# Optimization experiments

Measured on AMD Instinct MI355X. Metric: run time of the kernel, lower is better.

The kernel has to match this reference:

```python
import jax, jax.numpy as jnp
import numpy as np

HEAD = 8


def setup_inputs() -> dict:
    key0 = jax.random.key(0)
    ks = jax.random.split(key0, 16)
    B, K, RD, NH = 16, 1024, 1024, 1024
    s = 0.02
    inp = {
        "v": jax.random.normal(ks[0], (B, K, RD), jnp.float32),
        "key": jax.random.normal(ks[1], (B, K, RD), jnp.float32),
        "query": jax.random.normal(ks[2], (B, K, RD), jnp.float32),
        "mask": jax.random.randint(ks[3], (B, 1, 1, K), 0, 2).astype(bool),
        # FCNet([relation_dim, num_hid], act='') == Linear(relation_dim, num_hid)
        "Wq": jax.random.normal(ks[4], (RD, NH), jnp.float32) * s,
        "bq": jnp.zeros((NH,), jnp.float32),
        "Wk": jax.random.normal(ks[5], (RD, NH), jnp.float32) * s,
        "bk": jnp.zeros((NH,), jnp.float32),
        "Wv": jax.random.normal(ks[6], (RD, NH), jnp.float32) * s,
        "bv": jnp.zeros((NH,), jnp.float32),
        "Wm": jax.random.normal(ks[7], (NH, NH), jnp.float32) * s,
        "bm": jnp.zeros((NH,), jnp.float32),
    }
    return inp


def reference(v, key, query, mask, Wq, bq, Wk, bk, Wv, bv, Wm, bm):
    B, K, _ = v.shape
    NH = Wq.shape[1]
    dk = NH // HEAD

    def split_heads(x):  # [B,K,NH] -> [B,H,K,dk]
        return x.reshape(B, K, HEAD, dk).transpose(0, 2, 1, 3)

    q = split_heads(query @ Wq + bq)
    k = split_heads(key @ Wk + bk)
    vv = split_heads(v @ Wv + bv)

    scores = jnp.einsum("bhqd,bhkd->bhqk", q, k) / jnp.sqrt(jnp.float32(dk))
    scores = jnp.where(mask, jnp.float32(-1e9), scores)
    att = jax.nn.softmax(scores, axis=-1)  # dropout is identity at eval
    atted = jnp.einsum("bhqk,bhkd->bhqd", att, vv)
    atted = atted.transpose(0, 2, 1, 3).reshape(B, K, NH)
    atted = atted @ Wm + bm
    return atted, att
```

## Files before the change

### kernel.cpp

```cpp
#include <hip/hip_runtime.h>

typedef unsigned short u16;
typedef __attribute__((ext_vector_type(8))) short short8;
typedef __attribute__((ext_vector_type(4))) float floatx4;

#define MFMA16(a, b, c) __builtin_amdgcn_mfma_f32_16x16x32_bf16(a, b, c, 0, 0, 0)

#define BB 16
#define KK 1024
#define NH 1024
#define HD 8
#define DK 128
#define ATT_OFF 16777216

typedef const __attribute__((address_space(1))) unsigned gl_u32;
typedef __attribute__((address_space(3))) unsigned lds_u32;

__device__ __forceinline__ u16 f2bf(float x) {
  unsigned u = __builtin_bit_cast(unsigned, x);
  u += 0x7fffu + ((u >> 16) & 1u);
  return (u16)(u >> 16);
}

__device__ __forceinline__ void gload16(const u16* g, u16* l) {
  __builtin_amdgcn_global_load_lds((gl_u32*)g, (lds_u32*)l, 16, 0, 0);
}

__global__ __launch_bounds__(256) void cast_bf16x8(const float* __restrict__ in,
                                                   u16* __restrict__ out) {
  const size_t i = ((size_t)blockIdx.x * 256 + threadIdx.x) * 8;
  float4 f0 = *(const float4*)(in + i);
  float4 f1 = *(const float4*)(in + i + 4);
  union { u16 u[8]; uint4 v; } p;
  p.u[0] = f2bf(f0.x); p.u[1] = f2bf(f0.y); p.u[2] = f2bf(f0.z); p.u[3] = f2bf(f0.w);
  p.u[4] = f2bf(f1.x); p.u[5] = f2bf(f1.y); p.u[6] = f2bf(f1.z); p.u[7] = f2bf(f1.w);
  *(uint4*)(out + i) = p.v;
}

__global__ __launch_bounds__(256) void tr_w(const float* __restrict__ in,
                                            u16* __restrict__ out) {
  __shared__ u16 t[32][36];
  const int tid = threadIdx.x;
  const int bx = blockIdx.x * 32;
  const int by = blockIdx.y * 32;
  const int r = tid >> 3, c4 = (tid & 7) * 4;
  float4 f = *(const float4*)(in + (size_t)(by + r) * 1024 + bx + c4);
  t[r][c4 + 0] = f2bf(f.x);
  t[r][c4 + 1] = f2bf(f.y);
  t[r][c4 + 2] = f2bf(f.z);
  t[r][c4 + 3] = f2bf(f.w);
  __syncthreads();
  union { u16 u[4]; uint2 v; } p;
#pragma unroll
  for (int i = 0; i < 4; i++) p.u[i] = t[c4 + i][r];
  *(uint2*)(out + (size_t)(bx + r) * 1024 + by + c4) = p.v;
}

__global__ __launch_bounds__(256) void tr_head(const u16* __restrict__ vvb,
                                               u16* __restrict__ vvT) {
  __shared__ u16 t[32][36];
  const int tid = threadIdx.x;
  const int bh = blockIdx.z, b = bh >> 3, h = bh & 7;
  const int i0 = blockIdx.x * 32, d0 = blockIdx.y * 32;
  const int r = tid >> 3, c4 = (tid & 7) * 4;
  union { u16 u[4]; uint2 v; } p;
  p.v = *(const uint2*)(vvb + (size_t)(b * KK + i0 + r) * NH + h * DK + d0 + c4);
  t[r][c4 + 0] = p.u[0];
  t[r][c4 + 1] = p.u[1];
  t[r][c4 + 2] = p.u[2];
  t[r][c4 + 3] = p.u[3];
  __syncthreads();
#pragma unroll
  for (int i = 0; i < 4; i++) p.u[i] = t[c4 + i][r];
  *(uint2*)(vvT + (size_t)(bh * DK + d0 + r) * KK + i0 + c4) = p.v;
}

__global__ __launch_bounds__(256, 2) void gemm_bt(
    const u16* __restrict__ A, const u16* __restrict__ Bt,
    const float* __restrict__ bias, u16* __restrict__ Cb, float* __restrict__ Cf,
    int Kd, int ldc, long long aBatch, long long btBatch,
    long long cBatchB, long long cBatchH) {
  __shared__ __align__(16) u16 As[128 * 32];
  __shared__ __align__(16) u16 Bs[128 * 32];
  const int tid = threadIdx.x;
  const int z = blockIdx.z;

  int bxs = blockIdx.x, bys = blockIdx.y;
  if (gridDim.x == 8 && gridDim.y == 128 && gridDim.z == 1) {
    const int flat = blockIdx.x + 8 * blockIdx.y;
    const int xcd = flat & 7, idx = flat >> 3;
    const int nflat = xcd * 128 + idx;
    bxs = nflat & 7;
    bys = nflat >> 3;
  }
  const int nBase = bxs * 128;
  const int mBase = bys * 128;

  const u16* Ab = A + (size_t)z * aBatch;
  const u16* Bb = Bt + (size_t)z * btBatch;
  const size_t cOff = (size_t)(z >> 3) * cBatchB + (size_t)(z & 7) * cBatchH;

  const int wid = tid >> 6, lane = tid & 63;
  const int wm = (wid & 1) * 64, wn = (wid >> 1) * 64;
  const int lm = lane & 15, lq = lane >> 4;

  const int rIn = lane >> 2;
  const int sSlot = (lane & 3) * 8;
  u16* aDst0 = &As[(wid * 2 + 0) * 512];
  u16* aDst1 = &As[(wid * 2 + 1) * 512];
  u16* bDst0 = &Bs[(wid * 2 + 0) * 512];
  u16* bDst1 = &Bs[(wid * 2 + 1) * 512];
  const u16* aSrc0 = Ab + (size_t)(mBase + (wid * 2 + 0) * 16 + rIn) * Kd + sSlot;
  const u16* aSrc1 = Ab + (size_t)(mBase + (wid * 2 + 1) * 16 + rIn) * Kd + sSlot;
  const u16* bSrc0 = Bb + (size_t)(nBase + (wid * 2 + 0) * 16 + rIn) * Kd + sSlot;
  const u16* bSrc1 = Bb + (size_t)(nBase + (wid * 2 + 1) * 16 + rIn) * Kd + sSlot;

  floatx4 acc[4][4] = {};

  for (int k0 = 0; k0 < Kd; k0 += 32) {
    gload16(aSrc0 + k0, aDst0);
    gload16(aSrc1 + k0, aDst1);
    gload16(bSrc0 + k0, bDst0);
    gload16(bSrc1 + k0, bDst1);
    __syncthreads();

    short8 af[4], bfr[4];
#pragma unroll
    for (int t = 0; t < 4; t++) {
      af[t]  = *(const short8*)&As[(wm + t * 16 + lm) * 32 + lq * 8];
      bfr[t] = *(const short8*)&Bs[(wn + t * 16 + lm) * 32 + lq * 8];
    }
#pragma unroll
    for (int i = 0; i < 4; i++)
#pragma unroll
      for (int j = 0; j < 4; j++)
        acc[i][j] = MFMA16(af[i], bfr[j], acc[i][j]);
    __syncthreads();
  }

#pragma unroll
  for (int i = 0; i < 4; i++) {
    const int rowL = wm + i * 16 + lq * 4;
#pragma unroll
    for (int j = 0; j < 4; j++) {
      const int col = nBase + wn + j * 16 + lm;
      const float bval = bias ? bias[col] : 0.0f;
      const size_t base = cOff + (size_t)(mBase + rowL) * ldc + col;
#pragma unroll
      for (int r = 0; r < 4; r++) {
        const float v = acc[i][j][r] + bval;
        if (Cb) Cb[base + (size_t)r * ldc] = f2bf(v);
        if (Cf) Cf[base + (size_t)r * ldc] = v;
      }
    }
  }
}

__global__ __launch_bounds__(256, 2) void scores_softmax_pv(
    const u16* __restrict__ qb, const u16* __restrict__ kb,
    const int* __restrict__ mask, const u16* __restrict__ vvT,
    float* __restrict__ att, u16* __restrict__ atp) {
  __shared__ __align__(16) u16 p_lds[16 * 1024];
  u16* msk16 = p_lds;
  float* redM = (float*)&p_lds[1024];
  float* redS = (float*)&p_lds[1152];
  const int tid = threadIdx.x;

  const int flat = blockIdx.x + 64 * blockIdx.y;
  const int xcd = flat & 7, idx = flat >> 3;
  const int bh = xcd * 16 + (idx >> 6);
  const int rowBlk = idx & 63;

  const int b = bh >> 3, h = bh & 7;
  const int wid = tid >> 6, lane = tid & 63;
  const int lm = lane & 15, lq = lane >> 4;
  const int rowG = rowBlk * 16;

  {
    int4 m = *(const int4*)(mask + (size_t)b * KK + tid * 4);
    msk16[tid * 4 + 0] = (u16)(m.x != 0);
    msk16[tid * 4 + 1] = (u16)(m.y != 0);
    msk16[tid * 4 + 2] = (u16)(m.z != 0);
    msk16[tid * 4 + 3] = (u16)(m.w != 0);
  }

  short8 qf[4];
  const u16* qp = qb + (size_t)(b * KK + rowG + lm) * NH + h * DK + lq * 8;
#pragma unroll
  for (int ks = 0; ks < 4; ks++) qf[ks] = *(const short8*)(qp + ks * 32);

  floatx4 acc[16] = {};
  const u16* kpB = kb + (size_t)(b * KK + wid * 256 + lm) * NH + h * DK + lq * 8;
#pragma unroll
  for (int jt = 0; jt < 16; jt++) {
    const u16* kp = kpB + (size_t)jt * 16 * NH;
    short8 k0 = *(const short8*)(kp + 0);
    short8 k1 = *(const short8*)(kp + 32);
    short8 k2 = *(const short8*)(kp + 64);
    short8 k3 = *(const short8*)(kp + 96);
    floatx4 a = acc[jt];
    a = MFMA16(qf[0], k0, a);
    a = MFMA16(qf[1], k1, a);
    a = MFMA16(qf[2], k2, a);
    a = MFMA16(qf[3], k3, a);
    acc[jt] = a;
  }
  __syncthreads();

  const float scale = 0.08838834764831845f;
  float mrow[4] = {-3e38f, -3e38f, -3e38f, -3e38f};
#pragma unroll
  for (int jt = 0; jt < 16; jt++) {
    const int col = wid * 256 + jt * 16 + lm;
    const bool mk = msk16[col] != 0;
#pragma unroll
    for (int r = 0; r < 4; r++) {
      float s = mk ? -1e9f : acc[jt][r] * scale;
      acc[jt][r] = s;
      mrow[r] = fmaxf(mrow[r], s);
    }
  }
#pragma unroll
  for (int off = 1; off < 16; off <<= 1)
#pragma unroll
    for (int r = 0; r < 4; r++) mrow[r] = fmaxf(mrow[r], __shfl_xor(mrow[r], off));
  if (lm == 0) {
#pragma unroll
    for (int r = 0; r < 4; r++) redM[wid * 16 + lq * 4 + r] = mrow[r];
  }
  __syncthreads();
#pragma unroll
  for (int r = 0; r < 4; r++)
    mrow[r] = fmaxf(fmaxf(redM[0 + lq * 4 + r], redM[16 + lq * 4 + r]),
                    fmaxf(redM[32 + lq * 4 + r], redM[48 + lq * 4 + r]));

  float srow[4] = {0.f, 0.f, 0.f, 0.f};
#pragma unroll
  for (int jt = 0; jt < 16; jt++)
#pragma unroll
    for (int r = 0; r < 4; r++) {
      float e = __expf(acc[jt][r] - mrow[r]);
      acc[jt][r] = e;
      srow[r] += e;
    }
#pragma unroll
  for (int off = 1; off < 16; off <<= 1)
#pragma unroll
    for (int r = 0; r < 4; r++) srow[r] += __shfl_xor(srow[r], off);
  if (lm == 0) {
#pragma unroll
    for (int r = 0; r < 4; r++) redS[wid * 16 + lq * 4 + r] = srow[r];
  }
  __syncthreads();
#pragma unroll
  for (int r = 0; r < 4; r++) {
    float s = redS[0 + lq * 4 + r] + redS[16 + lq * 4 + r] +
              redS[32 + lq * 4 + r] + redS[48 + lq * 4 + r];
    srow[r] = 1.0f / s;
  }
  __syncthreads();

#pragma unroll
  for (int r = 0; r < 4; r++) {
    const int row = lq * 4 + r;
    float* attRow = att + ((size_t)bh * KK + rowG + row) * KK;
#pragma unroll
    for (int jt = 0; jt < 16; jt++) {
      const int col = wid * 256 + jt * 16 + lm;
      const float p = acc[jt][r] * srow[r];
      __builtin_nontemporal_store(p, attRow + col);
      p_lds[(row * 1024 + col) ^ ((row & 7) << 3)] = f2bf(p);
    }
  }
  __syncthreads();

  floatx4 pacc0 = {}, pacc1 = {}, pacc2 = {}, pacc3 = {};
  const u16* vBase = vvT + (size_t)bh * DK * KK + (size_t)(wid * 32 + lm) * KK + lq * 8;
#pragma unroll 4
  for (int k0 = 0; k0 < 512; k0 += 32) {
    short8 pfa = *(const short8*)&p_lds[(lm * 1024 + k0 + lq * 8) ^ ((lm & 7) << 3)];
    short8 pfb = *(const short8*)&p_lds[(lm * 1024 + 512 + k0 + lq * 8) ^ ((lm & 7) << 3)];
    short8 v0a = *(const short8*)(vBase + k0);
    short8 v1a = *(const short8*)(vBase + 16 * KK + k0);
    short8 v0b = *(const short8*)(vBase + 512 + k0);
    short8 v1b = *(const short8*)(vBase + 16 * KK + 512 + k0);
    pacc0 = MFMA16(pfa, v0a, pacc0);
    pacc1 = MFMA16(pfa, v1a, pacc1);
    pacc2 = MFMA16(pfb, v0b, pacc2);
    pacc3 = MFMA16(pfb, v1b, pacc3);
  }
  floatx4 o0 = pacc0 + pacc2;
  floatx4 o1 = pacc1 + pacc3;

#pragma unroll
  for (int r = 0; r < 4; r++) {
    const int row = rowG + lq * 4 + r;
    atp[(size_t)(b * KK + row) * NH + h * DK + wid * 32 + 0 + lm] = f2bf(o0[r]);
    atp[(size_t)(b * KK + row) * NH + h * DK + wid * 32 + 16 + lm] = f2bf(o1[r]);
  }
}

extern "C" void kernel_launch(void* const* d_in, const int* in_sizes, int n_in,
                              void* d_out, int out_size, void* d_ws, size_t ws_size,
                              hipStream_t stream) {
  const float* v     = (const float*)d_in[0];
  const float* key   = (const float*)d_in[1];
  const float* query = (const float*)d_in[2];
  const int*   mask  = (const int*)d_in[3];
  const float* Wq = (const float*)d_in[4];
  const float* bq = (const float*)d_in[5];
  const float* Wk = (const float*)d_in[6];
  const float* bk = (const float*)d_in[7];
  const float* Wv = (const float*)d_in[8];
  const float* bv = (const float*)d_in[9];
  const float* Wm = (const float*)d_in[10];
  const float* bm = (const float*)d_in[11];

  float* atted = (float*)d_out;
  float* att   = atted + (size_t)ATT_OFF;

  char* ws = (char*)d_ws;
  u16* qb   = (u16*)(ws + 0);
  u16* kb   = (u16*)(ws + 33554432ll);
  u16* vvb  = (u16*)(ws + 67108864ll);
  u16* vvT  = (u16*)(ws + 100663296ll);
  u16* atp  = (u16*)(ws + 134217728ll);
  u16* WqT  = (u16*)(ws + 167772160ll);
  u16* WkT  = (u16*)(ws + 169869312ll);
  u16* WvT  = (u16*)(ws + 171966464ll);
  u16* WmT  = (u16*)(ws + 174063616ll);

  u16* cq = (u16*)att;
  u16* ck = cq + 16777216;
  u16* cv = ck + 16777216;

  cast_bf16x8<<<8192, 256, 0, stream>>>(query, cq);
  cast_bf16x8<<<8192, 256, 0, stream>>>(key, ck);
  cast_bf16x8<<<8192, 256, 0, stream>>>(v, cv);

  tr_w<<<dim3(32, 32), 256, 0, stream>>>(Wq, WqT);
  tr_w<<<dim3(32, 32), 256, 0, stream>>>(Wk, WkT);
  tr_w<<<dim3(32, 32), 256, 0, stream>>>(Wv, WvT);
  tr_w<<<dim3(32, 32), 256, 0, stream>>>(Wm, WmT);

  gemm_bt<<<dim3(8, 128, 1), 256, 0, stream>>>(cq, WqT, bq, qb, nullptr,
                                               1024, 1024, 0, 0, 0, 0);
  gemm_bt<<<dim3(8, 128, 1), 256, 0, stream>>>(ck, WkT, bk, kb, nullptr,
                                               1024, 1024, 0, 0, 0, 0);
  gemm_bt<<<dim3(8, 128, 1), 256, 0, stream>>>(cv, WvT, bv, vvb, nullptr,
                                               1024, 1024, 0, 0, 0, 0);

  tr_head<<<dim3(32, 4, 128), 256, 0, stream>>>(vvb, vvT);

  scores_softmax_pv<<<dim3(64, 128), 256, 0, stream>>>(qb, kb, mask, vvT, att, atp);

  gemm_bt<<<dim3(8, 128, 1), 256, 0, stream>>>(atp, WmT, bm, nullptr, atted,
                                               1024, 1024, 0, 0, 0, 0);
}
```

Before: 1.337 ms.

## Double-buffer GEMM LDS, prefetch K/V fragments, batch cast and QKV launches

Double-buffers the GEMM shared-memory tiles so the next K-slice's global-to-LDS loads are issued before the current slice is consumed, leaving one barrier per iteration. The scores and PV phases now register-prefetch K and V fragments four steps ahead to hide global latency. The three cast kernels and the three QKV projection GEMMs are each merged into a single launch via a grid dimension, which cuts launch count and gives larger grids. The costs are doubled LDS use per GEMM block and higher register pressure from the prefetch buffers, which could reduce occupancy.

```diff
diff --git a/kernel.cpp b/kernel.cpp
--- a/kernel.cpp
+++ b/kernel.cpp
@@ -26,8 +26,12 @@
   __builtin_amdgcn_global_load_lds((gl_u32*)g, (lds_u32*)l, 16, 0, 0);
 }
 
-__global__ __launch_bounds__(256) void cast_bf16x8(const float* __restrict__ in,
-                                                   u16* __restrict__ out) {
+__global__ __launch_bounds__(256) void cast3_bf16x8(
+    const float* __restrict__ i0, const float* __restrict__ i1,
+    const float* __restrict__ i2, u16* __restrict__ o0, u16* __restrict__ o1,
+    u16* __restrict__ o2) {
+  const float* in = blockIdx.y == 0 ? i0 : (blockIdx.y == 1 ? i1 : i2);
+  u16* out = blockIdx.y == 0 ? o0 : (blockIdx.y == 1 ? o1 : o2);
   const size_t i = ((size_t)blockIdx.x * 256 + threadIdx.x) * 8;
   float4 f0 = *(const float4*)(in + i);
   float4 f1 = *(const float4*)(in + i + 4);
@@ -75,60 +79,46 @@
   *(uint2*)(vvT + (size_t)(bh * DK + d0 + r) * KK + i0 + c4) = p.v;
 }
 
-__global__ __launch_bounds__(256, 2) void gemm_bt(
-    const u16* __restrict__ A, const u16* __restrict__ Bt,
+__device__ __forceinline__ void gemm_body(
+    const u16* __restrict__ Ab, const u16* __restrict__ Bb,
     const float* __restrict__ bias, u16* __restrict__ Cb, float* __restrict__ Cf,
-    int Kd, int ldc, long long aBatch, long long btBatch,
-    long long cBatchB, long long cBatchH) {
-  __shared__ __align__(16) u16 As[128 * 32];
-  __shared__ __align__(16) u16 Bs[128 * 32];
+    const int Kd, const int ldc, const int nBase, const int mBase) {
+  __shared__ __align__(16) u16 As[2][128 * 32];
+  __shared__ __align__(16) u16 Bs[2][128 * 32];
   const int tid = threadIdx.x;
-  const int z = blockIdx.z;
-
-  int bxs = blockIdx.x, bys = blockIdx.y;
-  if (gridDim.x == 8 && gridDim.y == 128 && gridDim.z == 1) {
-    const int flat = blockIdx.x + 8 * blockIdx.y;
-    const int xcd = flat & 7, idx = flat >> 3;
-    const int nflat = xcd * 128 + idx;
-    bxs = nflat & 7;
-    bys = nflat >> 3;
-  }
-  const int nBase = bxs * 128;
-  const int mBase = bys * 128;
-
-  const u16* Ab = A + (size_t)z * aBatch;
-  const u16* Bb = Bt + (size_t)z * btBatch;
-  const size_t cOff = (size_t)(z >> 3) * cBatchB + (size_t)(z & 7) * cBatchH;
-
   const int wid = tid >> 6, lane = tid & 63;
   const int wm = (wid & 1) * 64, wn = (wid >> 1) * 64;
   const int lm = lane & 15, lq = lane >> 4;
-
   const int rIn = lane >> 2;
   const int sSlot = (lane & 3) * 8;
-  u16* aDst0 = &As[(wid * 2 + 0) * 512];
-  u16* aDst1 = &As[(wid * 2 + 1) * 512];
-  u16* bDst0 = &Bs[(wid * 2 + 0) * 512];
-  u16* bDst1 = &Bs[(wid * 2 + 1) * 512];
-  const u16* aSrc0 = Ab + (size_t)(mBase + (wid * 2 + 0) * 16 + rIn) * Kd + sSlot;
-  const u16* aSrc1 = Ab + (size_t)(mBase + (wid * 2 + 1) * 16 + rIn) * Kd + sSlot;
-  const u16* bSrc0 = Bb + (size_t)(nBase + (wid * 2 + 0) * 16 + rIn) * Kd + sSlot;
-  const u16* bSrc1 = Bb + (size_t)(nBase + (wid * 2 + 1) * 16 + rIn) * Kd + sSlot;
+
+  const u16* aS0 = Ab + (size_t)(mBase + (wid * 2 + 0) * 16 + rIn) * Kd + sSlot;
+  const u16* aS1 = Ab + (size_t)(mBase + (wid * 2 + 1) * 16 + rIn) * Kd + sSlot;
+  const u16* bS0 = Bb + (size_t)(nBase + (wid * 2 + 0) * 16 + rIn) * Kd + sSlot;
+  const u16* bS1 = Bb + (size_t)(nBase + (wid * 2 + 1) * 16 + rIn) * Kd + sSlot;
 
   floatx4 acc[4][4] = {};
 
+  gload16(aS0, &As[0][(wid * 2 + 0) * 512]);
+  gload16(aS1, &As[0][(wid * 2 + 1) * 512]);
+  gload16(bS0, &Bs[0][(wid * 2 + 0) * 512]);
+  gload16(bS1, &Bs[0][(wid * 2 + 1) * 512]);
+  __syncthreads();
+
+  int cur = 0;
   for (int k0 = 0; k0 < Kd; k0 += 32) {
-    gload16(aSrc0 + k0, aDst0);
-    gload16(aSrc1 + k0, aDst1);
-    gload16(bSrc0 + k0, bDst0);
-    gload16(bSrc1 + k0, bDst1);
-    __syncthreads();
-
+    const int nxt = cur ^ 1;
+    if (k0 + 32 < Kd) {
+      gload16(aS0 + k0 + 32, &As[nxt][(wid * 2 + 0) * 512]);
+      gload16(aS1 + k0 + 32, &As[nxt][(wid * 2 + 1) * 512]);
+      gload16(bS0 + k0 + 32, &Bs[nxt][(wid * 2 + 0) * 512]);
+      gload16(bS1 + k0 + 32, &Bs[nxt][(wid * 2 + 1) * 512]);
+    }
     short8 af[4], bfr[4];
 #pragma unroll
     for (int t = 0; t < 4; t++) {
-      af[t]  = *(const short8*)&As[(wm + t * 16 + lm) * 32 + lq * 8];
-      bfr[t] = *(const short8*)&Bs[(wn + t * 16 + lm) * 32 + lq * 8];
+      af[t]  = *(const short8*)&As[cur][(wm + t * 16 + lm) * 32 + lq * 8];
+      bfr[t] = *(const short8*)&Bs[cur][(wn + t * 16 + lm) * 32 + lq * 8];
     }
 #pragma unroll
     for (int i = 0; i < 4; i++)
@@ -136,6 +126,7 @@
       for (int j = 0; j < 4; j++)
         acc[i][j] = MFMA16(af[i], bfr[j], acc[i][j]);
     __syncthreads();
+    cur = nxt;
   }
 
 #pragma unroll
@@ -145,7 +136,7 @@
     for (int j = 0; j < 4; j++) {
       const int col = nBase + wn + j * 16 + lm;
       const float bval = bias ? bias[col] : 0.0f;
-      const size_t base = cOff + (size_t)(mBase + rowL) * ldc + col;
+      const size_t base = (size_t)(mBase + rowL) * ldc + col;
 #pragma unroll
       for (int r = 0; r < 4; r++) {
         const float v = acc[i][j][r] + bval;
@@ -154,6 +145,36 @@
       }
     }
   }
+}
+
+__device__ __forceinline__ int2 swz_grid() {
+  const int flat = blockIdx.x + 8 * blockIdx.y;
+  const int xcd = flat & 7, idx = flat >> 3;
+  const int nflat = xcd * 128 + idx;
+  return make_int2((nflat & 7) * 128, (nflat >> 3) * 128);
+}
+
+__global__ __launch_bounds__(256, 2) void gemm_bt(
+    const u16* __restrict__ A, const u16* __restrict__ Bt,
+    const float* __restrict__ bias, u16* __restrict__ Cb, float* __restrict__ Cf) {
+  int2 nm = swz_grid();
+  gemm_body(A, Bt, bias, Cb, Cf, 1024, 1024, nm.x, nm.y);
+}
+
+__global__ __launch_bounds__(256, 2) void gemm_qkv(
+    const u16* __restrict__ A0, const u16* __restrict__ A1,
+    const u16* __restrict__ A2, const u16* __restrict__ B0,
+    const u16* __restrict__ B1, const u16* __restrict__ B2,
+    const float* __restrict__ b0, const float* __restrict__ b1,
+    const float* __restrict__ b2, u16* __restrict__ C0, u16* __restrict__ C1,
+    u16* __restrict__ C2) {
+  const int z = blockIdx.z;
+  const u16* A = z == 0 ? A0 : (z == 1 ? A1 : A2);
+  const u16* B = z == 0 ? B0 : (z == 1 ? B1 : B2);
+  const float* bias = z == 0 ? b0 : (z == 1 ? b1 : b2);
+  u16* C = z == 0 ? C0 : (z == 1 ? C1 : C2);
+  int2 nm = swz_grid();
+  gemm_body(A, B, bias, C, nullptr, 1024, 1024, nm.x, nm.y);
 }
 
 __global__ __launch_bounds__(256, 2) void scores_softmax_pv(
@@ -191,18 +212,31 @@
 
   floatx4 acc[16] = {};
   const u16* kpB = kb + (size_t)(b * KK + wid * 256 + lm) * NH + h * DK + lq * 8;
+  short8 kf[4][4];
+#pragma unroll
+  for (int p = 0; p < 4; p++) {
+    const u16* kp = kpB + (size_t)p * 16 * NH;
+    kf[p][0] = *(const short8*)(kp + 0);
+    kf[p][1] = *(const short8*)(kp + 32);
+    kf[p][2] = *(const short8*)(kp + 64);
+    kf[p][3] = *(const short8*)(kp + 96);
+  }
 #pragma unroll
   for (int jt = 0; jt < 16; jt++) {
-    const u16* kp = kpB + (size_t)jt * 16 * NH;
-    short8 k0 = *(const short8*)(kp + 0);
-    short8 k1 = *(const short8*)(kp + 32);
-    short8 k2 = *(const short8*)(kp + 64);
-    short8 k3 = *(const short8*)(kp + 96);
+    const int slot = jt & 3;
+    short8 c0 = kf[slot][0], c1 = kf[slot][1], c2 = kf[slot][2], c3 = kf[slot][3];
+    if (jt + 4 < 16) {
+      const u16* kp = kpB + (size_t)(jt + 4) * 16 * NH;
+      kf[slot][0] = *(const short8*)(kp + 0);
+      kf[slot][1] = *(const short8*)(kp + 32);
+      kf[slot][2] = *(const short8*)(kp + 64);
+      kf[slot][3] = *(const short8*)(kp + 96);
+    }
     floatx4 a = acc[jt];
-    a = MFMA16(qf[0], k0, a);
-    a = MFMA16(qf[1], k1, a);
-    a = MFMA16(qf[2], k2, a);
-    a = MFMA16(qf[3], k3, a);
+    a = MFMA16(qf[0], c0, a);
+    a = MFMA16(qf[1], c1, a);
+    a = MFMA16(qf[2], c2, a);
+    a = MFMA16(qf[3], c3, a);
     acc[jt] = a;
   }
   __syncthreads();
@@ -276,18 +310,28 @@
 
   floatx4 pacc0 = {}, pacc1 = {}, pacc2 = {}, pacc3 = {};
   const u16* vBase = vvT + (size_t)bh * DK * KK + (size_t)(wid * 32 + lm) * KK + lq * 8;
-#pragma unroll 4
-  for (int k0 = 0; k0 < 512; k0 += 32) {
-    short8 pfa = *(const short8*)&p_lds[(lm * 1024 + k0 + lq * 8) ^ ((lm & 7) << 3)];
-    short8 pfb = *(const short8*)&p_lds[(lm * 1024 + 512 + k0 + lq * 8) ^ ((lm & 7) << 3)];
-    short8 v0a = *(const short8*)(vBase + k0);
-    short8 v1a = *(const short8*)(vBase + 16 * KK + k0);
-    short8 v0b = *(const short8*)(vBase + 512 + k0);
-    short8 v1b = *(const short8*)(vBase + 16 * KK + 512 + k0);
-    pacc0 = MFMA16(pfa, v0a, pacc0);
-    pacc1 = MFMA16(pfa, v1a, pacc1);
-    pacc2 = MFMA16(pfb, v0b, pacc2);
-    pacc3 = MFMA16(pfb, v1b, pacc3);
+  short8 vf[4][2];
+#pragma unroll
+  for (int p = 0; p < 4; p++) {
+    vf[p][0] = *(const short8*)(vBase + p * 32);
+    vf[p][1] = *(const short8*)(vBase + 16 * KK + p * 32);
+  }
+#pragma unroll
+  for (int s = 0; s < 32; s++) {
+    const int slot = s & 3;
+    short8 v0 = vf[slot][0], v1 = vf[slot][1];
+    if (s + 4 < 32) {
+      vf[slot][0] = *(const short8*)(vBase + (s + 4) * 32);
+      vf[slot][1] = *(const short8*)(vBase + 16 * KK + (s + 4) * 32);
+    }
+    short8 pf = *(const short8*)&p_lds[(lm * 1024 + s * 32 + lq * 8) ^ ((lm & 7) << 3)];
+    if (s & 1) {
+      pacc2 = MFMA16(pf, v0, pacc2);
+      pacc3 = MFMA16(pf, v1, pacc3);
+    } else {
+      pacc0 = MFMA16(pf, v0, pacc0);
+      pacc1 = MFMA16(pf, v1, pacc1);
+    }
   }
   floatx4 o0 = pacc0 + pacc2;
   floatx4 o1 = pacc1 + pacc3;
@@ -334,26 +378,19 @@
   u16* ck = cq + 16777216;
   u16* cv = ck + 16777216;
 
-  cast_bf16x8<<<8192, 256, 0, stream>>>(query, cq);
-  cast_bf16x8<<<8192, 256, 0, stream>>>(key, ck);
-  cast_bf16x8<<<8192, 256, 0, stream>>>(v, cv);
+  cast3_bf16x8<<<dim3(8192, 3), 256, 0, stream>>>(query, key, v, cq, ck, cv);
 
   tr_w<<<dim3(32, 32), 256, 0, stream>>>(Wq, WqT);
   tr_w<<<dim3(32, 32), 256, 0, stream>>>(Wk, WkT);
   tr_w<<<dim3(32, 32), 256, 0, stream>>>(Wv, WvT);
   tr_w<<<dim3(32, 32), 256, 0, stream>>>(Wm, WmT);
 
-  gemm_bt<<<dim3(8, 128, 1), 256, 0, stream>>>(cq, WqT, bq, qb, nullptr,
-                                               1024, 1024, 0, 0, 0, 0);
-  gemm_bt<<<dim3(8, 128, 1), 256, 0, stream>>>(ck, WkT, bk, kb, nullptr,
-                                               1024, 1024, 0, 0, 0, 0);
-  gemm_bt<<<dim3(8, 128, 1), 256, 0, stream>>>(cv, WvT, bv, vvb, nullptr,
-                                               1024, 1024, 0, 0, 0, 0);
+  gemm_qkv<<<dim3(8, 128, 3), 256, 0, stream>>>(cq, ck, cv, WqT, WkT, WvT,
+                                                bq, bk, bv, qb, kb, vvb);
 
   tr_head<<<dim3(32, 4, 128), 256, 0, stream>>>(vvb, vvT);
 
   scores_softmax_pv<<<dim3(64, 128), 256, 0, stream>>>(qb, kb, mask, vvT, att, atp);
 
-  gemm_bt<<<dim3(8, 128, 1), 256, 0, stream>>>(atp, WmT, bm, nullptr, atted,
-                                               1024, 1024, 0, 0, 0, 0);
-}
+  gemm_bt<<<dim3(8, 128), 256, 0, stream>>>(atp, WmT, bm, nullptr, atted);
+}
```

Measured after the change: 1.329 ms. Within noise of the previous version (-0.6%).
